# Optimization experiments

Hardware: AMD Instinct MI355X
Metric: run time of the kernel (lower is better)

Reference implementation:

```python
import jax, jax.numpy as jnp
import numpy as np

EPS = 1e-5


def clin(xr, xi, Wr, Wi, br, bi):
    # complex linear layer: (xr + i xi) @ (Wr + i Wi) + (br + i bi)
    yr = xr @ Wr - xi @ Wi + br
    yi = xr @ Wi + xi @ Wr + bi
    return yr, yi


def setup_inputs() -> dict:
    key = jax.random.key(0)
    ks = jax.random.split(key, 16)
    B, N, DE, DV = 4, 256, 128, 64
    s_in = 1.0 / np.sqrt(DE)
    s_p = 1.0 / np.sqrt(DV)
    f32 = jnp.float32
    inp = {
        'Z_q': jax.random.normal(ks[0], (B, 2, N, DE), f32),
        'Z_k': jax.random.normal(ks[1], (B, 2, N, DE), f32),
        'Z_v': jax.random.normal(ks[2], (B, 2, N, DE), f32),
        't_measure_all': jnp.tile(jnp.arange(N + 1, dtype=f32) * 0.01, (B, 1)),
        'Wq_r': jax.random.normal(ks[3], (DE, DV), f32) * s_in,
        'Wq_i': jax.random.normal(ks[4], (DE, DV), f32) * s_in,
        'bq_r': jnp.zeros((DV,), f32), 'bq_i': jnp.zeros((DV,), f32),
        'Wk_r': jax.random.normal(ks[5], (DE, DV), f32) * s_in,
        'Wk_i': jax.random.normal(ks[6], (DE, DV), f32) * s_in,
        'bk_r': jnp.zeros((DV,), f32), 'bk_i': jnp.zeros((DV,), f32),
        'Wv_r': jax.random.normal(ks[7], (DE, DV), f32) * s_in,
        'Wv_i': jax.random.normal(ks[8], (DE, DV), f32) * s_in,
        'bv_r': jnp.zeros((DV,), f32), 'bv_i': jnp.zeros((DV,), f32),
        'Wp_r': jax.random.normal(ks[9], (DV, DE), f32) * s_p,
        'Wp_i': jax.random.normal(ks[10], (DV, DE), f32) * s_p,
        'bp_r': jnp.zeros((DE,), f32), 'bp_i': jnp.zeros((DE,), f32),
        'lambda1': jax.random.normal(ks[11], (2, DV // 2), f32),
        'lambda_Omega_sqrt': jax.random.normal(ks[12], (DV,), f32) / DV,
        'lambda_Gamma_sqrt': jax.random.normal(ks[13], (DV,), f32) / DV,
        'noise_floor': jnp.array(1.0, f32),
        'tau': jnp.array(1.0, f32),
        'nu': jnp.array(1.0, f32),
        'eta_param': jnp.zeros((DV,), f32),
    }
    return inp


def reference(Z_q, Z_k, Z_v, t_measure_all,
              Wq_r, Wq_i, bq_r, bq_i, Wk_r, Wk_i, bk_r, bk_i,
              Wv_r, Wv_i, bv_r, bv_i, Wp_r, Wp_i, bp_r, bp_i,
              lambda1, lambda_Omega_sqrt, lambda_Gamma_sqrt,
              noise_floor, tau, nu, eta_param):
    N = Z_q.shape[2]
    # complex projections (B, N, d)
    Qr, Qi = clin(Z_q[:, 0], Z_q[:, 1], Wq_r, Wq_i, bq_r, bq_i)
    Kr_, Ki_ = clin(Z_k[:, 0], Z_k[:, 1], Wk_r, Wk_i, bk_r, bk_i)
    Vr, Vi = clin(Z_v[:, 0], Z_v[:, 1], Wv_r, Wv_i, bv_r, bv_i)
    # state-transition eigenvalues: stable conjugate pairs
    re = jnp.concatenate([-lambda1[0] ** 2, -lambda1[0] ** 2])  # (d_v,), Re<=0
    im = jnp.concatenate([lambda1[1], -lambda1[1]])             # (d_v,)
    lam_Om = lambda_Omega_sqrt ** 2
    lam_Ga = lambda_Gamma_sqrt ** 2 + EPS
    # pairwise complex exponential kernel exp(lambda * (t_i - t_j))
    t = t_measure_all[0, :-1]                       # (N,)
    dt = t[:, None] - t[None, :]                    # (N, N)
    amp = jnp.exp(re[None, None, :] * dt[:, :, None])
    ph = im[None, None, :] * dt[:, :, None]
    Ker = amp * jnp.cos(ph)                          # (N, N, d_v)
    Kei = amp * jnp.sin(ph)
    # propagated value estimates Z_hat_ij = exp(lam dt_ij) * V_j
    Zhr = Ker[None] * Vr[:, None] - Kei[None] * Vi[:, None]  # (B, N, N, d_v)
    Zhi = Ker[None] * Vi[:, None] + Kei[None] * Vr[:, None]
    # residuals R_ij = Q_i - exp(lam dt_ij) * K_j
    Rr = Qr[:, :, None, :] - (Ker[None] * Kr_[:, None] - Kei[None] * Ki_[:, None])
    Ri = Qi[:, :, None, :] - (Ker[None] * Ki_[:, None] + Kei[None] * Kr_[:, None])
    # per-pair covariance (OU-process propagation of measurement + process noise)
    adt = jnp.abs(dt)[:, :, None]
    exp2 = jnp.exp(2.0 * re * adt)                   # (N, N, d_v)
    Vij = lam_Ga * exp2 + lam_Om * (exp2 - 1.0) / (2.0 * (re - EPS))
    # mahalanobis distance and attention scores
    mah = (Rr ** 2 + Ri ** 2) / (Vij[None] + lam_Ga)          # (B, N, N, d_v)
    dist_sum = jnp.abs(nu) * jnp.sum(mah, axis=3, keepdims=True)
    base = Vij[None] * (noise_floor + dist_sum + EPS)
    scores = -jnp.abs(tau) * jnp.log(base)
    mask = jnp.tril(jnp.ones((N, N), bool))
    scores = jnp.where(mask[None, :, :, None], scores, -jnp.inf)
    Qij = jax.nn.softmax(scores, axis=2)             # normalize over j
    m = mask[None, :, :, None].astype(Zhr.dtype)
    Zhr = Zhr * m
    Zhi = Zhi * m
    est_vr = jnp.einsum('bijd,bijd->bid', Qij, Zhr)
    est_vi = jnp.einsum('bijd,bijd->bid', Qij, Zhi)
    # gated residual mix (double sigmoid as in source)
    eta = jax.nn.sigmoid(eta_param)
    g = jax.nn.sigmoid(eta)
    elr = (1.0 - eta) * Vr + g * est_vr
    eli = (1.0 - eta) * Vi + g * est_vi
    # one-step-ahead prediction via matrix exponential exp(lambda * h)
    h = t[1] - t[0]
    ma = jnp.exp(re * h)
    mr, mi = ma * jnp.cos(im * h), ma * jnp.sin(im * h)
    ppr = mr * elr - mi * eli
    ppi = mr * eli + mi * elr
    outr, outi = clin(ppr, ppi, Wp_r, Wp_i, bp_r, bp_i)
    est_latent = jnp.stack([elr, eli], axis=1)       # (B, 2, N, d_v)
    out = jnp.stack([outr, outi], axis=1)            # (B, 2, N, d_e)
    Zhat = jnp.stack([Zhr, Zhi], axis=1)             # (B, 2, N, N, d_v)
    lambda_h = jnp.stack([re, im])                   # (2, d_v)
    return est_latent, out, Qij, Zhat, lambda_h
```

## Files before the change

kernel.cpp:

```cpp
#include <hip/hip_runtime.h>
#include <math.h>

#define B_ 4
#define N_ 256
#define DE_ 128
#define DV_ 64
#define EPS_ 1e-5f

typedef __attribute__((ext_vector_type(4))) float f32x4;

__device__ __forceinline__ f32x4 ld4(const float* p) { return *(const f32x4*)p; }
__device__ __forceinline__ void st4(float* p, f32x4 v) { *(f32x4*)p = v; }
__device__ __forceinline__ void nt4(float* p, f32x4 v) { __builtin_nontemporal_store(v, (f32x4*)p); }

#define OFF_ETA   0
#define OFF_G     64
#define OFF_MR    128
#define OFF_MI    192
#define OFF_KER   256
#define OFF_KEI   (OFF_KER + N_*DV_)
#define OFF_A     (OFF_KEI + N_*DV_)
#define OFF_INV   (OFF_A + N_*DV_)
#define OFF_QR    (OFF_INV + N_*DV_)
#define OFF_QI    (OFF_QR + B_*N_*DV_)
#define OFF_KR    (OFF_QI + B_*N_*DV_)
#define OFF_KI    (OFF_KR + B_*N_*DV_)
#define OFF_VR    (OFF_KI + B_*N_*DV_)
#define OFF_VI    (OFF_VR + B_*N_*DV_)

#define OUT_EL    0
#define OUT_OUT   (B_*2*N_*DV_)
#define OUT_QIJ   (OUT_OUT + B_*2*N_*DE_)
#define OUT_ZHAT  (OUT_QIJ + B_*N_*N_*DV_)
#define OUT_LAMH  (OUT_ZHAT + (size_t)B_*2*N_*N_*DV_)

__global__ __launch_bounds__(256) void k_pre(
    const float* __restrict__ Zq, const float* __restrict__ Zk, const float* __restrict__ Zv,
    const float* __restrict__ Wqr, const float* __restrict__ Wqi,
    const float* __restrict__ bqr, const float* __restrict__ bqi,
    const float* __restrict__ Wkr, const float* __restrict__ Wki,
    const float* __restrict__ bkr, const float* __restrict__ bki,
    const float* __restrict__ Wvr, const float* __restrict__ Wvi,
    const float* __restrict__ bvr, const float* __restrict__ bvi,
    const float* __restrict__ t,  const float* __restrict__ lam1,
    const float* __restrict__ lOm, const float* __restrict__ lGa,
    const float* __restrict__ eta_p, const float* __restrict__ tau_p,
    float* __restrict__ ws, float* __restrict__ out)
{
    const int tid = (int)threadIdx.x;
    const int wv = tid >> 6;
    const int d = tid & 63;

    if (blockIdx.x >= 256) {
        const int idx = (int)blockIdx.x - 256;
        const int delta = idx * 4 + wv;

        const float l0 = lam1[d & 31];
        const float re = -l0 * l0;
        const float im = (d < 32) ? lam1[32 + d] : -lam1[d];

        const float lo = lOm[d];
        const float lam_Om = lo * lo;
        const float lg_ = lGa[d];
        const float lam_Ga = lg_ * lg_ + EPS_;
        const float tau_a = fabsf(tau_p[0]);

        const float t0 = t[0];
        const float dt = t[delta] - t0;

        const float amp = expf(re * dt);
        const float ph  = im * dt;
        const int td = delta * DV_ + d;
        ws[OFF_KER + td] = amp * cosf(ph);
        ws[OFF_KEI + td] = amp * sinf(ph);

        const float e2  = expf(2.0f * re * dt);
        const float vij = lam_Ga * e2 + lam_Om * (e2 - 1.0f) / (2.0f * (re - EPS_));
        ws[OFF_A   + td] = expf(-tau_a * logf(vij));
        ws[OFF_INV + td] = 1.0f / (vij + lam_Ga);

        if (delta == 0) {
            const float eta = 1.0f / (1.0f + expf(-eta_p[d]));
            const float g   = 1.0f / (1.0f + expf(-eta));
            ws[OFF_ETA + d] = eta;
            ws[OFF_G   + d] = g;
            const float h  = t[1] - t0;
            const float ma = expf(re * h);
            ws[OFF_MR + d] = ma * cosf(im * h);
            ws[OFF_MI + d] = ma * sinf(im * h);
            out[OUT_LAMH + d]       = re;
            out[OUT_LAMH + DV_ + d] = im;
        }
        return;
    }

    const int row0 = (int)blockIdx.x * 4;
    const int b = row0 >> 8;
    const int n0 = row0 & (N_ - 1);

    __shared__ float x[4][6][DE_];
    #pragma unroll
    for (int it = 0; it < 3; ++it) {
        const int v = tid + it * 256;
        const int seg = v >> 5;
        const int pos = v & 31;
        const int r = seg & 3;
        const int a = seg >> 2;
        const int m = a >> 1;
        const int c = a & 1;
        const float* src = (m == 0) ? Zq : ((m == 1) ? Zk : Zv);
        const f32x4 val = ld4(src + ((size_t)(b*2 + c)*N_ + (n0 + r))*DE_ + pos*4);
        st4(&x[r][a][pos*4], val);
    }
    __syncthreads();

    const int row = row0 + wv;
    float aqr = 0.f, aqi = 0.f, akr = 0.f, aki = 0.f, avr = 0.f, avi = 0.f;
    #pragma unroll 8
    for (int k = 0; k < DE_; ++k) {
        const float xqr = x[wv][0][k], xqi = x[wv][1][k];
        const float xkr = x[wv][2][k], xki = x[wv][3][k];
        const float xvr = x[wv][4][k], xvi = x[wv][5][k];
        float wr, wi;
        wr = Wqr[k*DV_ + d]; wi = Wqi[k*DV_ + d];
        aqr += xqr*wr - xqi*wi; aqi += xqr*wi + xqi*wr;
        wr = Wkr[k*DV_ + d]; wi = Wki[k*DV_ + d];
        akr += xkr*wr - xki*wi; aki += xkr*wi + xki*wr;
        wr = Wvr[k*DV_ + d]; wi = Wvi[k*DV_ + d];
        avr += xvr*wr - xvi*wi; avi += xvr*wi + xvi*wr;
    }
    const int o = row * DV_ + d;
    ws[OFF_QR + o] = aqr + bqr[d];
    ws[OFF_QI + o] = aqi + bqi[d];
    ws[OFF_KR + o] = akr + bkr[d];
    ws[OFF_KI + o] = aki + bki[d];
    ws[OFF_VR + o] = avr + bvr[d];
    ws[OFF_VI + o] = avi + bvi[d];
}

__global__ __launch_bounds__(256) void k_main2(
    const float* __restrict__ ws, float* __restrict__ out,
    const float* __restrict__ Wpr, const float* __restrict__ Wpi,
    const float* __restrict__ bpr, const float* __restrict__ bpi,
    const float* __restrict__ nf_p, const float* __restrict__ tau_p,
    const float* __restrict__ nu_p)
{
    const int vb = (int)blockIdx.x;
    const int b = vb & 3;
    const int i = (N_ - 1) - (vb >> 2);
    const int row = b * N_ + i;
    const int tid = (int)threadIdx.x;
    const int wv = tid >> 6;
    const int l = tid & 63;
    const int g = l >> 4;
    const int q16 = l & 15;
    const int dq = q16 * 4;

    __shared__ float wl[N_];
    __shared__ f32x4 redS[4][16];
    __shared__ f32x4 redR[4][16];
    __shared__ f32x4 redI[4][16];
    __shared__ float ppr_s[DV_], ppi_s[DV_];

    const float nf    = nf_p[0];
    const float tau_a = fabsf(tau_p[0]);
    const float nu_a  = fabsf(nu_p[0]);

    const f32x4 qr4 = ld4(ws + OFF_QR + row*DV_ + dq);
    const f32x4 qi4 = ld4(ws + OFF_QI + row*DV_ + dq);

    const int nfull = (i + 1) >> 2;
    const int tail  = (i + 1) & 3;
    const f32x4 z4 = {0.f,0.f,0.f,0.f};

    float* qij = out + OUT_QIJ + (size_t)row * N_ * DV_;
    float* zro = out + OUT_ZHAT + ((size_t)(b*2+0)*N_ + i) * N_ * DV_;
    float* zio = out + OUT_ZHAT + ((size_t)(b*2+1)*N_ + i) * N_ * DV_;

    f32x4 s4  = {0.f,0.f,0.f,0.f};
    f32x4 evr = {0.f,0.f,0.f,0.f};
    f32x4 evi = {0.f,0.f,0.f,0.f};
    #pragma unroll 2
    for (int T = wv; T < nfull; T += 4) {
        const int j = 4*T + g;
        const int o = j*DV_ + dq;
        const int td = (i - j)*DV_ + dq;
        const f32x4 ker = ld4(ws + OFF_KER + td);
        const f32x4 kei = ld4(ws + OFF_KEI + td);
        const f32x4 vnv = ld4(ws + OFF_INV + td);
        const f32x4 a4  = ld4(ws + OFF_A   + td);
        const int kj = (b*N_ + j)*DV_ + dq;
        const f32x4 kr = ld4(ws + OFF_KR + kj);
        const f32x4 ki = ld4(ws + OFF_KI + kj);
        const f32x4 vr = ld4(ws + OFF_VR + kj);
        const f32x4 vi = ld4(ws + OFF_VI + kj);
        const f32x4 rr = qr4 - (ker*kr - kei*ki);
        const f32x4 ri = qi4 - (ker*ki + kei*kr);
        const f32x4 mah = (rr*rr + ri*ri) * vnv;
        float ds = mah[0] + mah[1] + mah[2] + mah[3];
        ds += __shfl_xor(ds, 1);
        ds += __shfl_xor(ds, 2);
        ds += __shfl_xor(ds, 4);
        ds += __shfl_xor(ds, 8);
        const float wj = expf(-tau_a * logf(nf + nu_a*ds + EPS_));
        if (q16 == 0) wl[j] = wj;
        const f32x4 zr = ker*vr - kei*vi;
        const f32x4 zi = ker*vi + kei*vr;
        nt4(zro + o, zr);
        nt4(zio + o, zi);
        const f32x4 qn = a4 * wj;
        s4  += qn;
        evr += qn * zr;
        evi += qn * zi;
    }
    if (tail && ((nfull & 3) == wv)) {
        const int j = 4*nfull + g;
        const int o = j*DV_ + dq;
        const bool act = (g < tail);
        const int td = (act ? (i - j) : 0)*DV_ + dq;
        const f32x4 ker = ld4(ws + OFF_KER + td);
        const f32x4 kei = ld4(ws + OFF_KEI + td);
        const f32x4 vnv = ld4(ws + OFF_INV + td);
        const f32x4 a4  = ld4(ws + OFF_A   + td);
        const int kj = (b*N_ + (act ? j : 0))*DV_ + dq;
        const f32x4 kr = ld4(ws + OFF_KR + kj);
        const f32x4 ki = ld4(ws + OFF_KI + kj);
        const f32x4 vr = ld4(ws + OFF_VR + kj);
        const f32x4 vi = ld4(ws + OFF_VI + kj);
        const f32x4 rr = qr4 - (ker*kr - kei*ki);
        const f32x4 ri = qi4 - (ker*ki + kei*kr);
        const f32x4 mah = (rr*rr + ri*ri) * vnv;
        float ds = mah[0] + mah[1] + mah[2] + mah[3];
        ds += __shfl_xor(ds, 1);
        ds += __shfl_xor(ds, 2);
        ds += __shfl_xor(ds, 4);
        ds += __shfl_xor(ds, 8);
        if (act) {
            const float wj = expf(-tau_a * logf(nf + nu_a*ds + EPS_));
            if (q16 == 0) wl[j] = wj;
            const f32x4 zr = ker*vr - kei*vi;
            const f32x4 zi = ker*vi + kei*vr;
            nt4(zro + o, zr);
            nt4(zio + o, zi);
            const f32x4 qn = a4 * wj;
            s4  += qn;
            evr += qn * zr;
            evi += qn * zi;
        } else {
            nt4(zro + o, z4);
            nt4(zio + o, z4);
        }
    }
    {
        const int jz0 = 4 * (nfull + (tail ? 1 : 0));
        const int nq = (N_ - jz0) * 16;
        for (int u = tid; u < nq; u += 256) {
            const int o = jz0*DV_ + u*4;
            nt4(zro + o, z4);
            nt4(zio + o, z4);
        }
    }

    #pragma unroll
    for (int mask = 16; mask <= 32; mask <<= 1) {
        #pragma unroll
        for (int c = 0; c < 4; ++c) {
            s4[c]  += __shfl_xor(s4[c],  mask);
            evr[c] += __shfl_xor(evr[c], mask);
            evi[c] += __shfl_xor(evi[c], mask);
        }
    }
    if (g == 0) { redS[wv][q16] = s4; redR[wv][q16] = evr; redI[wv][q16] = evi; }
    __syncthreads();
    const f32x4 Z = redS[0][q16] + redS[1][q16] + redS[2][q16] + redS[3][q16];
    const f32x4 one = {1.f,1.f,1.f,1.f};
    const f32x4 invZ = one / Z;

    #pragma unroll 2
    for (int T = wv; T < nfull; T += 4) {
        const int j = 4*T + g;
        const int o = j*DV_ + dq;
        const int td = (i - j)*DV_ + dq;
        const f32x4 q4 = ld4(ws + OFF_A + td) * wl[j] * invZ;
        nt4(qij + o, q4);
    }
    if (tail && ((nfull & 3) == wv)) {
        const int j = 4*nfull + g;
        const int o = j*DV_ + dq;
        if (g < tail) {
            const int td = (i - j)*DV_ + dq;
            const f32x4 q4 = ld4(ws + OFF_A + td) * wl[j] * invZ;
            nt4(qij + o, q4);
        } else {
            nt4(qij + o, z4);
        }
    }
    {
        const int jz0 = 4 * (nfull + (tail ? 1 : 0));
        const int nq = (N_ - jz0) * 16;
        for (int u = tid; u < nq; u += 256) {
            nt4(qij + jz0*DV_ + u*4, z4);
        }
    }

    if (tid < 16) {
        const f32x4 Zt = redS[0][tid] + redS[1][tid] + redS[2][tid] + redS[3][tid];
        const f32x4 iZ = one / Zt;
        const f32x4 Evr = (redR[0][tid] + redR[1][tid] + redR[2][tid] + redR[3][tid]) * iZ;
        const f32x4 Evi = (redI[0][tid] + redI[1][tid] + redI[2][tid] + redI[3][tid]) * iZ;
        const int dq2 = tid * 4;
        const f32x4 vr  = ld4(ws + OFF_VR + row*DV_ + dq2);
        const f32x4 vi  = ld4(ws + OFF_VI + row*DV_ + dq2);
        const f32x4 eta = ld4(ws + OFF_ETA + dq2);
        const f32x4 gg  = ld4(ws + OFF_G + dq2);
        const f32x4 elr = (1.0f - eta)*vr + gg*Evr;
        const f32x4 eli = (1.0f - eta)*vi + gg*Evi;
        st4(out + OUT_EL + ((size_t)(b*2+0)*N_ + i)*DV_ + dq2, elr);
        st4(out + OUT_EL + ((size_t)(b*2+1)*N_ + i)*DV_ + dq2, eli);
        const f32x4 mr = ld4(ws + OFF_MR + dq2);
        const f32x4 mi = ld4(ws + OFF_MI + dq2);
        st4(ppr_s + dq2, mr*elr - mi*eli);
        st4(ppi_s + dq2, mr*eli + mi*elr);
    }
    __syncthreads();

    if (tid < DE_) {
        const int e = tid;
        float ar = bpr[e], ai = bpi[e];
        #pragma unroll 8
        for (int dd = 0; dd < DV_; ++dd) {
            const float wr = Wpr[dd*DE_ + e], wi = Wpi[dd*DE_ + e];
            const float r = ppr_s[dd], im = ppi_s[dd];
            ar += r*wr - im*wi;
            ai += r*wi + im*wr;
        }
        out[OUT_OUT + ((size_t)(b*2+0)*N_ + i)*DE_ + e] = ar;
        out[OUT_OUT + ((size_t)(b*2+1)*N_ + i)*DE_ + e] = ai;
    }
}

extern "C" void kernel_launch(void* const* d_in, const int* in_sizes, int n_in,
                              void* d_out, int out_size, void* d_ws, size_t ws_size,
                              hipStream_t stream)
{
    const float* Zq   = (const float*)d_in[0];
    const float* Zk   = (const float*)d_in[1];
    const float* Zv   = (const float*)d_in[2];
    const float* t    = (const float*)d_in[3];
    const float* Wqr  = (const float*)d_in[4];
    const float* Wqi  = (const float*)d_in[5];
    const float* bqr  = (const float*)d_in[6];
    const float* bqi  = (const float*)d_in[7];
    const float* Wkr  = (const float*)d_in[8];
    const float* Wki  = (const float*)d_in[9];
    const float* bkr  = (const float*)d_in[10];
    const float* bki  = (const float*)d_in[11];
    const float* Wvr  = (const float*)d_in[12];
    const float* Wvi  = (const float*)d_in[13];
    const float* bvr  = (const float*)d_in[14];
    const float* bvi  = (const float*)d_in[15];
    const float* Wpr  = (const float*)d_in[16];
    const float* Wpi  = (const float*)d_in[17];
    const float* bpr  = (const float*)d_in[18];
    const float* bpi  = (const float*)d_in[19];
    const float* lam1 = (const float*)d_in[20];
    const float* lOm  = (const float*)d_in[21];
    const float* lGa  = (const float*)d_in[22];
    const float* nf   = (const float*)d_in[23];
    const float* tau  = (const float*)d_in[24];
    const float* nu   = (const float*)d_in[25];
    const float* etap = (const float*)d_in[26];

    float* ws  = (float*)d_ws;
    float* out = (float*)d_out;

    k_pre<<<256 + 64, 256, 0, stream>>>(Zq, Zk, Zv,
                                        Wqr, Wqi, bqr, bqi,
                                        Wkr, Wki, bkr, bki,
                                        Wvr, Wvi, bvr, bvi,
                                        t, lam1, lOm, lGa, etap, tau, ws, out);
    k_main2<<<B_*N_, 256, 0, stream>>>(ws, out, Wpr, Wpi, bpr, bpi, nf, tau, nu);
}
```

Before: 68.25 us.

## Offload Zhat and masked Qij zero writes to extra evenly-split blocks

The Zhat output, including its masked zeros, and the zero-fill of the upper triangle of Qij move out of the per-row attention blocks into extra blocks appended to the same grid. Each extra block writes a fixed contiguous chunk of the flattened output, recomputing Zhat from the kernel and V tensors in the workspace. This is meant to remove the load imbalance of the triangular per-row work, where early rows mostly wrote zeros and later rows mostly wrote data. The cost is recomputing the complex products for Zhat and using regular rather than nontemporal stores in the new blocks.

```diff
diff --git a/kernel.cpp b/kernel.cpp
--- a/kernel.cpp
+++ b/kernel.cpp
@@ -6,6 +6,11 @@
 #define DE_ 128
 #define DV_ 64
 #define EPS_ 1e-5f
+
+#define NEXP_Z 1232
+#define NEXP_Q 304
+#define CH_Z   6810
+#define CH_Q   13798
 
 typedef __attribute__((ext_vector_type(4))) float f32x4;
 
@@ -146,22 +151,61 @@
     const float* __restrict__ nu_p)
 {
     const int vb = (int)blockIdx.x;
+    const int tid = (int)threadIdx.x;
+
+    __shared__ float wl[N_];
+    __shared__ f32x4 redS[4][16];
+    __shared__ f32x4 redR[4][16];
+    __shared__ f32x4 redI[4][16];
+    __shared__ float ppr_s[DV_], ppi_s[DV_];
+
+    if (vb >= 1024) {
+        const f32x4 z4 = {0.f,0.f,0.f,0.f};
+        const int eb = vb - 1024;
+        if (eb < NEXP_Z) {
+            long long u0 = (long long)eb * CH_Z;
+            long long ue = u0 + CH_Z; if (ue > 8388608LL) ue = 8388608LL;
+            for (long long u = u0 + tid; u < ue; u += 256) {
+                const int ui  = (int)u;
+                const int dqi = ui & 15;
+                const int j   = (ui >> 4) & 255;
+                const int ii  = (ui >> 12) & 255;
+                const int bc  = ui >> 20;
+                const int bb  = bc >> 1, cc = bc & 1;
+                const int delta = ii - j;
+                const int td = (delta > 0 ? delta : 0)*DV_ + dqi*4;
+                const f32x4 ker = ld4(ws + OFF_KER + td);
+                const f32x4 kei = ld4(ws + OFF_KEI + td);
+                const int kj = (bb*N_ + j)*DV_ + dqi*4;
+                const f32x4 vr = ld4(ws + OFF_VR + kj);
+                const f32x4 vi = ld4(ws + OFF_VI + kj);
+                f32x4 z = (cc == 0) ? (ker*vr - kei*vi) : (ker*vi + kei*vr);
+                if (delta < 0) z = z4;
+                st4(out + OUT_ZHAT + (size_t)u*4, z);
+            }
+        } else {
+            const int qb = eb - NEXP_Z;
+            long long u0 = (long long)qb * CH_Q;
+            long long ue = u0 + CH_Q; if (ue > 4194304LL) ue = 4194304LL;
+            for (long long u = u0 + tid; u < ue; u += 256) {
+                const int ui = (int)u;
+                const int j  = (ui >> 4) & 255;
+                const int ii = (ui >> 12) & 255;
+                if (j > ii) st4(out + OUT_QIJ + (size_t)u*4, z4);
+            }
+        }
+        return;
+    }
+
     const int b = vb & 3;
     const int i = (N_ - 1) - (vb >> 2);
     const int row = b * N_ + i;
-    const int tid = (int)threadIdx.x;
     const int wv = tid >> 6;
     const int l = tid & 63;
     const int g = l >> 4;
     const int q16 = l & 15;
     const int dq = q16 * 4;
 
-    __shared__ float wl[N_];
-    __shared__ f32x4 redS[4][16];
-    __shared__ f32x4 redR[4][16];
-    __shared__ f32x4 redI[4][16];
-    __shared__ float ppr_s[DV_], ppi_s[DV_];
-
     const float nf    = nf_p[0];
     const float tau_a = fabsf(tau_p[0]);
     const float nu_a  = fabsf(nu_p[0]);
@@ -171,11 +215,8 @@
 
     const int nfull = (i + 1) >> 2;
     const int tail  = (i + 1) & 3;
-    const f32x4 z4 = {0.f,0.f,0.f,0.f};
 
     float* qij = out + OUT_QIJ + (size_t)row * N_ * DV_;
-    float* zro = out + OUT_ZHAT + ((size_t)(b*2+0)*N_ + i) * N_ * DV_;
-    float* zio = out + OUT_ZHAT + ((size_t)(b*2+1)*N_ + i) * N_ * DV_;
 
     f32x4 s4  = {0.f,0.f,0.f,0.f};
     f32x4 evr = {0.f,0.f,0.f,0.f};
@@ -183,7 +224,6 @@
     #pragma unroll 2
     for (int T = wv; T < nfull; T += 4) {
         const int j = 4*T + g;
-        const int o = j*DV_ + dq;
         const int td = (i - j)*DV_ + dq;
         const f32x4 ker = ld4(ws + OFF_KER + td);
         const f32x4 kei = ld4(ws + OFF_KEI + td);
@@ -206,8 +246,6 @@
         if (q16 == 0) wl[j] = wj;
         const f32x4 zr = ker*vr - kei*vi;
         const f32x4 zi = ker*vi + kei*vr;
-        nt4(zro + o, zr);
-        nt4(zio + o, zi);
         const f32x4 qn = a4 * wj;
         s4  += qn;
         evr += qn * zr;
@@ -215,7 +253,6 @@
     }
     if (tail && ((nfull & 3) == wv)) {
         const int j = 4*nfull + g;
-        const int o = j*DV_ + dq;
         const bool act = (g < tail);
         const int td = (act ? (i - j) : 0)*DV_ + dq;
         const f32x4 ker = ld4(ws + OFF_KER + td);
@@ -240,24 +277,10 @@
             if (q16 == 0) wl[j] = wj;
             const f32x4 zr = ker*vr - kei*vi;
             const f32x4 zi = ker*vi + kei*vr;
-            nt4(zro + o, zr);
-            nt4(zio + o, zi);
             const f32x4 qn = a4 * wj;
             s4  += qn;
             evr += qn * zr;
             evi += qn * zi;
-        } else {
-            nt4(zro + o, z4);
-            nt4(zio + o, z4);
-        }
-    }
-    {
-        const int jz0 = 4 * (nfull + (tail ? 1 : 0));
-        const int nq = (N_ - jz0) * 16;
-        for (int u = tid; u < nq; u += 256) {
-            const int o = jz0*DV_ + u*4;
-            nt4(zro + o, z4);
-            nt4(zio + o, z4);
         }
     }
 
@@ -284,23 +307,12 @@
         const f32x4 q4 = ld4(ws + OFF_A + td) * wl[j] * invZ;
         nt4(qij + o, q4);
     }
-    if (tail && ((nfull & 3) == wv)) {
+    if (tail && ((nfull & 3) == wv) && (g < tail)) {
         const int j = 4*nfull + g;
         const int o = j*DV_ + dq;
-        if (g < tail) {
-            const int td = (i - j)*DV_ + dq;
-            const f32x4 q4 = ld4(ws + OFF_A + td) * wl[j] * invZ;
-            nt4(qij + o, q4);
-        } else {
-            nt4(qij + o, z4);
-        }
-    }
-    {
-        const int jz0 = 4 * (nfull + (tail ? 1 : 0));
-        const int nq = (N_ - jz0) * 16;
-        for (int u = tid; u < nq; u += 256) {
-            nt4(qij + jz0*DV_ + u*4, z4);
-        }
+        const int td = (i - j)*DV_ + dq;
+        const f32x4 q4 = ld4(ws + OFF_A + td) * wl[j] * invZ;
+        nt4(qij + o, q4);
     }
 
     if (tid < 16) {
@@ -379,5 +391,5 @@
                                         Wkr, Wki, bkr, bki,
                                         Wvr, Wvi, bvr, bvi,
                                         t, lam1, lOm, lGa, etap, tau, ws, out);
-    k_main2<<<B_*N_, 256, 0, stream>>>(ws, out, Wpr, Wpi, bpr, bpi, nf, tau, nu);
+    k_main2<<<1024 + NEXP_Z + NEXP_Q, 256, 0, stream>>>(ws, out, Wpr, Wpi, bpr, bpi, nf, tau, nu);
 }
```

Measured after the change: 75.98 us. +11.3%, slower.
